# Performance work log

Hardware: AMD Instinct MI355X
Metric: run time of the kernel (lower is better)

Reference implementation:

```python
import jax, jax.numpy as jnp
import numpy as np

B, H, S, DK = 4, 16, 2048, 64


def setup_inputs() -> dict:
    key = jax.random.key(0)
    kq, kk, kv, km = jax.random.split(key, 4)
    Q = jax.random.normal(kq, (B, H, S, DK), dtype=jnp.float32)
    K = jax.random.normal(kk, (B, H, S, DK), dtype=jnp.float32)
    V = jax.random.normal(kv, (B, H, S, DK), dtype=jnp.float32)
    mask = (jax.random.uniform(km, (B, 1, S, S)) > 0.1).astype(jnp.float32)
    return {"Q": Q, "K": K, "V": V, "mask": mask}


def reference(Q, K, V, mask):
    d_k = Q.shape[-1]
    # unnormalized exp scores (no max subtraction), multiplicative mask
    scores = jnp.exp(jnp.einsum("bhqd,bhkd->bhqk", Q, K) / jnp.sqrt(jnp.float32(d_k)))
    scores = scores * mask
    attn = scores / (jnp.sum(scores, axis=-1, keepdims=True) + 1e-8)
    return jnp.einsum("bhqk,bhkd->bhqd", attn, V)
```

## Files before the change

kernel.cpp:

```cpp
#include <hip/hip_runtime.h>

namespace {
constexpr int S  = 2048;
constexpr int D  = 64;
constexpr int BQ = 128;
constexpr int BK = 64;
constexpr int NT = 512;
constexpr int NKT = S / BK;
constexpr int PSTR = 72;

typedef short bf16x8 __attribute__((ext_vector_type(8)));
typedef float f32x4  __attribute__((ext_vector_type(4)));

__device__ inline unsigned short bf16c(float x) {
  __bf16 h = (__bf16)x;
  return __builtin_bit_cast(unsigned short, h);
}
__device__ inline unsigned pk2(float a, float b) {
  return (unsigned)bf16c(a) | ((unsigned)bf16c(b) << 16);
}
__device__ inline void gld_lds16(const void* g, void* l) {
  __builtin_amdgcn_global_load_lds(
      (const __attribute__((address_space(1))) unsigned int*)g,
      (__attribute__((address_space(3))) unsigned int*)l, 16, 0, 0);
}

__global__ __launch_bounds__(256) void prep_k(const float* __restrict__ K,
                                              unsigned short* __restrict__ Kws) {
  int gid = blockIdx.x * 256 + threadIdx.x;
  int row = gid >> 3;
  int g   = gid & 7;
  const float* src = K + (size_t)row * 64 + g * 8;
  float4 a = *(const float4*)src;
  float4 b = *(const float4*)(src + 4);
  uint4 w;
  w.x = pk2(a.x, a.y); w.y = pk2(a.z, a.w);
  w.z = pk2(b.x, b.y); w.w = pk2(b.z, b.w);
  *(uint4*)(Kws + (size_t)row * 64 + ((g ^ (row & 7)) * 8)) = w;
}

__global__ __launch_bounds__(256) void prep_v(const float* __restrict__ V,
                                              unsigned short* __restrict__ Vws) {
  __shared__ float tl[64 * 68];
  const int t = threadIdx.x;
  const size_t tile = blockIdx.x;
  const float* src = V + tile * (64 * 64);
#pragma unroll
  for (int rep = 0; rep < 4; ++rep) {
    int idx = t + rep * 256;
    int row = idx >> 4, d4 = idx & 15;
    float4 v = *(const float4*)(src + row * 64 + d4 * 4);
    *(float4*)(tl + row * 68 + d4 * 4) = v;
  }
  __syncthreads();
  unsigned short* dstT = Vws + tile * (64 * 64);
#pragma unroll
  for (int rep = 0; rep < 2; ++rep) {
    int d  = (t & 31) + rep * 32;
    int kg = t >> 5;
    float x[8];
#pragma unroll
    for (int j = 0; j < 8; ++j) x[j] = tl[(kg * 8 + j) * 68 + d];
    uint4 w;
    w.x = pk2(x[0], x[1]); w.y = pk2(x[2], x[3]);
    w.z = pk2(x[4], x[5]); w.w = pk2(x[6], x[7]);
    *(uint4*)(dstT + d * 64 + ((kg ^ (d & 7)) * 8)) = w;
  }
}

__global__ __launch_bounds__(256) void prep_m(const float* __restrict__ M,
                                              unsigned char* __restrict__ M2) {
  size_t gid = (size_t)blockIdx.x * 256 + threadIdx.x;
  int n16  = gid & 15;
  int quad = (gid >> 4) & 3;
  size_t rest = gid >> 6;
  int qband = rest & 127;
  int kt    = (rest >> 7) & 31;
  int b     = rest >> 12;
  unsigned wds[4];
#pragma unroll
  for (int r = 0; r < 4; ++r) {
    int q = qband * 16 + quad * 4 + r;
    const float* src = M + ((size_t)b * S + q) * S + kt * 64 + n16;
    unsigned w = 0;
#pragma unroll
    for (int nt = 0; nt < 4; ++nt)
      w |= (src[nt * 16] != 0.0f ? 1u : 0u) << (8 * nt);
    wds[r] = w;
  }
  uint4 out = make_uint4(wds[0], wds[1], wds[2], wds[3]);
  *(uint4*)(M2 + gid * 16) = out;
}

__global__ __launch_bounds__(NT, 6)
void attn3(const float* __restrict__ Qg, const unsigned char* __restrict__ M2,
           const unsigned short* __restrict__ Kws,
           const unsigned short* __restrict__ Vws,
           float* __restrict__ Og) {
  __shared__ __align__(16) unsigned short sK[2][BK * D];
  __shared__ __align__(16) unsigned short sV[2][BK * D];
  __shared__ __align__(16) unsigned short sP[BQ * PSTR];

  const int t    = threadIdx.x;
  const int wave = t >> 6;
  const int lane = t & 63;
  const int quad = lane >> 4;
  const int n16  = lane & 15;

  const int bh = blockIdx.y;
  const int b  = bh >> 4;
  const int q0 = blockIdx.x * BQ;
  const int qband = blockIdx.x * 8 + wave;

  const unsigned short* Kb = Kws + (size_t)bh * S * D;
  const unsigned short* Vb = Vws + (size_t)bh * S * D;
  const unsigned char* Mp = M2
      + ((((size_t)b * NKT) * 128 + qband) * 4 + quad) * 256 + n16 * 16;
  constexpr size_t MKT = (size_t)128 * 4 * 16 * 16;

  const float* Qb = Qg + ((size_t)bh * S + q0 + wave * 16) * D;
  bf16x8 aq[2];
#pragma unroll
  for (int ks = 0; ks < 2; ++ks) {
    const float* qp = Qb + n16 * D + ks * 32 + quad * 8;
    float4 x = *(const float4*)qp;
    float4 y = *(const float4*)(qp + 4);
    bf16x8 a;
    a[0] = (short)bf16c(x.x * 0.125f); a[1] = (short)bf16c(x.y * 0.125f);
    a[2] = (short)bf16c(x.z * 0.125f); a[3] = (short)bf16c(x.w * 0.125f);
    a[4] = (short)bf16c(y.x * 0.125f); a[5] = (short)bf16c(y.y * 0.125f);
    a[6] = (short)bf16c(y.z * 0.125f); a[7] = (short)bf16c(y.w * 0.125f);
    aq[ks] = a;
  }

  f32x4 o[4];
#pragma unroll
  for (int nt = 0; nt < 4; ++nt) o[nt] = (f32x4){0.f, 0.f, 0.f, 0.f};
  float rs[4] = {0.f, 0.f, 0.f, 0.f};
  uint4 mk[2];

  gld_lds16(Kb + wave * 512 + lane * 8, &sK[0][wave * 512]);
  gld_lds16(Vb + wave * 512 + lane * 8, &sV[0][wave * 512]);
  mk[0] = *(const uint4*)Mp;

#pragma unroll 2
  for (int kt = 0; kt < NKT; ++kt) {
    const int cur = kt & 1, nxt = cur ^ 1;
    __syncthreads();

    if (kt + 1 < NKT) {
      gld_lds16(Kb + (size_t)(kt + 1) * (BK * D) + wave * 512 + lane * 8,
                &sK[nxt][wave * 512]);
      gld_lds16(Vb + (size_t)(kt + 1) * (BK * D) + wave * 512 + lane * 8,
                &sV[nxt][wave * 512]);
      mk[nxt] = *(const uint4*)(Mp + (size_t)(kt + 1) * MKT);
    }

    f32x4 sc[4];
#pragma unroll
    for (int nt = 0; nt < 4; ++nt) {
      const int row = nt * 16 + n16, sw = row & 7;
      bf16x8 bk0 = *(const bf16x8*)(sK[cur] + row * 64 + ((quad) ^ sw) * 8);
      bf16x8 bk1 = *(const bf16x8*)(sK[cur] + row * 64 + ((quad + 4) ^ sw) * 8);
      sc[nt] = (f32x4){0.f, 0.f, 0.f, 0.f};
      sc[nt] = __builtin_amdgcn_mfma_f32_16x16x32_bf16(aq[0], bk0, sc[nt], 0, 0, 0);
      sc[nt] = __builtin_amdgcn_mfma_f32_16x16x32_bf16(aq[1], bk1, sc[nt], 0, 0, 0);
    }

    const unsigned mw[4] = {mk[cur].x, mk[cur].y, mk[cur].z, mk[cur].w};
#pragma unroll
    for (int nt = 0; nt < 4; ++nt)
#pragma unroll
      for (int r = 0; r < 4; ++r) {
        float m = (float)((mw[r] >> (8 * nt)) & 0xffu);
        float p = __expf(sc[nt][r]) * m;
        unsigned short u = bf16c(p);
        rs[r] += __builtin_bit_cast(float, (unsigned)u << 16);
        sP[(wave * 16 + quad * 4 + r) * PSTR + nt * 16 + n16] = u;
      }

    const int prow = wave * 16 + n16;
    bf16x8 ap0 = *(const bf16x8*)(sP + prow * PSTR + quad * 8);
    bf16x8 ap1 = *(const bf16x8*)(sP + prow * PSTR + 32 + quad * 8);
#pragma unroll
    for (int nt = 0; nt < 4; ++nt) {
      const int row = nt * 16 + n16, sw = row & 7;
      bf16x8 bv0 = *(const bf16x8*)(sV[cur] + row * 64 + ((quad) ^ sw) * 8);
      bf16x8 bv1 = *(const bf16x8*)(sV[cur] + row * 64 + ((quad + 4) ^ sw) * 8);
      o[nt] = __builtin_amdgcn_mfma_f32_16x16x32_bf16(ap0, bv0, o[nt], 0, 0, 0);
      o[nt] = __builtin_amdgcn_mfma_f32_16x16x32_bf16(ap1, bv1, o[nt], 0, 0, 0);
    }
  }

  float inv[4];
#pragma unroll
  for (int r = 0; r < 4; ++r) {
    float v = rs[r];
    v += __shfl_xor(v, 1);
    v += __shfl_xor(v, 2);
    v += __shfl_xor(v, 4);
    v += __shfl_xor(v, 8);
    inv[r] = 1.0f / (v + 1e-8f);
  }
  float* Ob = Og + ((size_t)bh * S + q0 + wave * 16) * D;
#pragma unroll
  for (int nt = 0; nt < 4; ++nt)
#pragma unroll
    for (int r = 0; r < 4; ++r)
      Ob[(size_t)(quad * 4 + r) * D + nt * 16 + n16] = o[nt][r] * inv[r];
}
}

extern "C" void kernel_launch(void* const* d_in, const int* in_sizes, int n_in,
                              void* d_out, int out_size, void* d_ws, size_t ws_size,
                              hipStream_t stream) {
  const float* Q = (const float*)d_in[0];
  const float* K = (const float*)d_in[1];
  const float* V = (const float*)d_in[2];
  const float* M = (const float*)d_in[3];
  float* O = (float*)d_out;

  unsigned short* Kws = (unsigned short*)d_ws;
  unsigned short* Vws = Kws + (size_t)64 * S * D;
  unsigned char*  M2  = (unsigned char*)(Vws + (size_t)64 * S * D);

  prep_k<<<dim3(64 * S * D / 8 / 256), 256, 0, stream>>>(K, Kws);
  prep_v<<<dim3(64 * NKT), 256, 0, stream>>>(V, Vws);
  prep_m<<<dim3(4 * NKT * 128 * 4 * 16 / 256), 256, 0, stream>>>(M, M2);
  attn3<<<dim3(S / BQ, 64), NT, 0, stream>>>(Q, M2, Kws, Vws, O);
}
```

Baseline: 292.1 us.

## Compute transposed S^T tiles to keep P in registers and double rows per wave

Swaps the MFMA operand order so the score tile comes out transposed, which lets the exp'd probabilities be packed directly into MFMA A/B operands. This removes the shared-memory P round-trip. Each wave now handles 32 query rows (BQ=256), so every K/V fragment read from LDS is reused twice. Row sums come from an MFMA against a ones vector instead of a shuffle reduction. exp2 with a pre-scaled Q replaces __expf, and the K swizzle and mask packing are reorganized to match the new fragment layout. The costs are higher register pressure (occupancy hint lowered to 4), fewer blocks, and mask loads that are no longer prefetched a tile ahead.

```diff
diff --git a/kernel.cpp b/kernel.cpp
--- a/kernel.cpp
+++ b/kernel.cpp
@@ -3,11 +3,10 @@
 namespace {
 constexpr int S  = 2048;
 constexpr int D  = 64;
-constexpr int BQ = 128;
+constexpr int BQ = 256;
 constexpr int BK = 64;
 constexpr int NT = 512;
 constexpr int NKT = S / BK;
-constexpr int PSTR = 72;
 
 typedef short bf16x8 __attribute__((ext_vector_type(8)));
 typedef float f32x4  __attribute__((ext_vector_type(4)));
@@ -23,6 +22,28 @@
   __builtin_amdgcn_global_load_lds(
       (const __attribute__((address_space(1))) unsigned int*)g,
       (__attribute__((address_space(3))) unsigned int*)l, 16, 0, 0);
+}
+#if __has_builtin(__builtin_amdgcn_exp2f)
+__device__ inline float exp2v(float x) { return __builtin_amdgcn_exp2f(x); }
+#else
+__device__ inline float exp2v(float x) { return __expf(x * 0.6931471805599453f); }
+#endif
+
+__device__ inline int kswz_of_row(int row) {
+  return ((row >> 3) & 3) | ((row & 1) << 2);
+}
+
+__device__ inline bf16x8 mk_pa(f32x4 s0, f32x4 s1, unsigned mw0, unsigned mw1) {
+  float p0 = exp2v(s0[0]) * (float)(mw0 & 0xffu);
+  float p1 = exp2v(s0[1]) * (float)((mw0 >> 8) & 0xffu);
+  float p2 = exp2v(s0[2]) * (float)((mw0 >> 16) & 0xffu);
+  float p3 = exp2v(s0[3]) * (float)(mw0 >> 24);
+  float p4 = exp2v(s1[0]) * (float)(mw1 & 0xffu);
+  float p5 = exp2v(s1[1]) * (float)((mw1 >> 8) & 0xffu);
+  float p6 = exp2v(s1[2]) * (float)((mw1 >> 16) & 0xffu);
+  float p7 = exp2v(s1[3]) * (float)(mw1 >> 24);
+  uint4 u = make_uint4(pk2(p0, p1), pk2(p2, p3), pk2(p4, p5), pk2(p6, p7));
+  return __builtin_bit_cast(bf16x8, u);
 }
 
 __global__ __launch_bounds__(256) void prep_k(const float* __restrict__ K,
@@ -36,7 +57,7 @@
   uint4 w;
   w.x = pk2(a.x, a.y); w.y = pk2(a.z, a.w);
   w.z = pk2(b.x, b.y); w.w = pk2(b.z, b.w);
-  *(uint4*)(Kws + (size_t)row * 64 + ((g ^ (row & 7)) * 8)) = w;
+  *(uint4*)(Kws + (size_t)row * 64 + ((g ^ kswz_of_row(row)) * 8)) = w;
 }
 
 __global__ __launch_bounds__(256) void prep_v(const float* __restrict__ V,
@@ -71,35 +92,37 @@
 __global__ __launch_bounds__(256) void prep_m(const float* __restrict__ M,
                                               unsigned char* __restrict__ M2) {
   size_t gid = (size_t)blockIdx.x * 256 + threadIdx.x;
-  int n16  = gid & 15;
-  int quad = (gid >> 4) & 3;
-  size_t rest = gid >> 6;
-  int qband = rest & 127;
-  int kt    = (rest >> 7) & 31;
-  int b     = rest >> 12;
+  int g    = (int)(gid & 1);
+  int lane = (int)((gid >> 1) & 63);
+  int qg   = (int)((gid >> 7) & 63);
+  int kt   = (int)((gid >> 13) & 31);
+  int b    = (int)(gid >> 18);
+  int n16  = lane & 15;
+  int quad = (lane >> 4) & 3;
+  int q = qg * 32 + g * 16 + n16;
+  const float* src = M + ((size_t)b * S + q) * S + kt * 64 + quad * 8;
   unsigned wds[4];
 #pragma unroll
-  for (int r = 0; r < 4; ++r) {
-    int q = qband * 16 + quad * 4 + r;
-    const float* src = M + ((size_t)b * S + q) * S + kt * 64 + n16;
-    unsigned w = 0;
-#pragma unroll
-    for (int nt = 0; nt < 4; ++nt)
-      w |= (src[nt * 16] != 0.0f ? 1u : 0u) << (8 * nt);
-    wds[r] = w;
-  }
-  uint4 out = make_uint4(wds[0], wds[1], wds[2], wds[3]);
-  *(uint4*)(M2 + gid * 16) = out;
-}
-
-__global__ __launch_bounds__(NT, 6)
+  for (int w = 0; w < 4; ++w) {
+    int ks = w >> 1, h = w & 1;
+    float4 v = *(const float4*)(src + ks * 32 + h * 4);
+    unsigned m = 0;
+    if (v.x != 0.0f) m |= 0x00000001u;
+    if (v.y != 0.0f) m |= 0x00000100u;
+    if (v.z != 0.0f) m |= 0x00010000u;
+    if (v.w != 0.0f) m |= 0x01000000u;
+    wds[w] = m;
+  }
+  *(uint4*)(M2 + gid * 16) = make_uint4(wds[0], wds[1], wds[2], wds[3]);
+}
+
+__global__ __launch_bounds__(NT, 4)
 void attn3(const float* __restrict__ Qg, const unsigned char* __restrict__ M2,
            const unsigned short* __restrict__ Kws,
            const unsigned short* __restrict__ Vws,
            float* __restrict__ Og) {
   __shared__ __align__(16) unsigned short sK[2][BK * D];
   __shared__ __align__(16) unsigned short sV[2][BK * D];
-  __shared__ __align__(16) unsigned short sP[BQ * PSTR];
 
   const int t    = threadIdx.x;
   const int wave = t >> 6;
@@ -110,104 +133,131 @@
   const int bh = blockIdx.y;
   const int b  = bh >> 4;
   const int q0 = blockIdx.x * BQ;
-  const int qband = blockIdx.x * 8 + wave;
+  const int qg = blockIdx.x * 8 + wave;
 
   const unsigned short* Kb = Kws + (size_t)bh * S * D;
   const unsigned short* Vb = Vws + (size_t)bh * S * D;
-  const unsigned char* Mp = M2
-      + ((((size_t)b * NKT) * 128 + qband) * 4 + quad) * 256 + n16 * 16;
-  constexpr size_t MKT = (size_t)128 * 4 * 16 * 16;
-
-  const float* Qb = Qg + ((size_t)bh * S + q0 + wave * 16) * D;
-  bf16x8 aq[2];
+  const unsigned char* Mp = M2 + (((size_t)b * NKT * 64 + qg) * 64 + lane) * 32;
+  constexpr size_t MKT = (size_t)64 * 64 * 32;
+
+  const int h2 = n16 >> 2, rr = n16 & 3;
+  const int kswz  = h2 | ((rr & 1) << 2);
+  const int koffA = (quad ^ kswz) * 8;
+  const int koffB = ((quad + 4) ^ kswz) * 8;
+  const int krow0 = (8 * h2 + rr) * 64;
+
+  const int sw = n16 & 7;
+  const int ga = (quad ^ sw) * 8;
+  const int gb = ((quad + 4) ^ sw) * 8;
+
+  constexpr float QS = 0.18033688011112042f;
+  const float* QbA = Qg + ((size_t)bh * S + q0 + wave * 32 + n16) * D;
+  bf16x8 aqA[2], aqB[2];
 #pragma unroll
   for (int ks = 0; ks < 2; ++ks) {
-    const float* qp = Qb + n16 * D + ks * 32 + quad * 8;
+    const float* qp = QbA + ks * 32 + quad * 8;
     float4 x = *(const float4*)qp;
     float4 y = *(const float4*)(qp + 4);
     bf16x8 a;
-    a[0] = (short)bf16c(x.x * 0.125f); a[1] = (short)bf16c(x.y * 0.125f);
-    a[2] = (short)bf16c(x.z * 0.125f); a[3] = (short)bf16c(x.w * 0.125f);
-    a[4] = (short)bf16c(y.x * 0.125f); a[5] = (short)bf16c(y.y * 0.125f);
-    a[6] = (short)bf16c(y.z * 0.125f); a[7] = (short)bf16c(y.w * 0.125f);
-    aq[ks] = a;
-  }
-
-  f32x4 o[4];
-#pragma unroll
-  for (int nt = 0; nt < 4; ++nt) o[nt] = (f32x4){0.f, 0.f, 0.f, 0.f};
-  float rs[4] = {0.f, 0.f, 0.f, 0.f};
-  uint4 mk[2];
+    a[0] = (short)bf16c(x.x * QS); a[1] = (short)bf16c(x.y * QS);
+    a[2] = (short)bf16c(x.z * QS); a[3] = (short)bf16c(x.w * QS);
+    a[4] = (short)bf16c(y.x * QS); a[5] = (short)bf16c(y.y * QS);
+    a[6] = (short)bf16c(y.z * QS); a[7] = (short)bf16c(y.w * QS);
+    aqA[ks] = a;
+    const float* qp2 = qp + 16 * D;
+    float4 x2 = *(const float4*)qp2;
+    float4 y2 = *(const float4*)(qp2 + 4);
+    bf16x8 a2;
+    a2[0] = (short)bf16c(x2.x * QS); a2[1] = (short)bf16c(x2.y * QS);
+    a2[2] = (short)bf16c(x2.z * QS); a2[3] = (short)bf16c(x2.w * QS);
+    a2[4] = (short)bf16c(y2.x * QS); a2[5] = (short)bf16c(y2.y * QS);
+    a2[6] = (short)bf16c(y2.z * QS); a2[7] = (short)bf16c(y2.w * QS);
+    aqB[ks] = a2;
+  }
+
+  bf16x8 ones;
+#pragma unroll
+  for (int i = 0; i < 8; ++i) ones[i] = (short)0x3F80;
+
+  f32x4 oA[4], oB[4];
+#pragma unroll
+  for (int nt = 0; nt < 4; ++nt) {
+    oA[nt] = (f32x4){0.f, 0.f, 0.f, 0.f};
+    oB[nt] = (f32x4){0.f, 0.f, 0.f, 0.f};
+  }
+  f32x4 rsA = (f32x4){0.f, 0.f, 0.f, 0.f};
+  f32x4 rsB = (f32x4){0.f, 0.f, 0.f, 0.f};
 
   gld_lds16(Kb + wave * 512 + lane * 8, &sK[0][wave * 512]);
   gld_lds16(Vb + wave * 512 + lane * 8, &sV[0][wave * 512]);
-  mk[0] = *(const uint4*)Mp;
 
 #pragma unroll 2
   for (int kt = 0; kt < NKT; ++kt) {
     const int cur = kt & 1, nxt = cur ^ 1;
     __syncthreads();
+
+    uint4 mkA = *(const uint4*)(Mp + (size_t)kt * MKT);
+    uint4 mkB = *(const uint4*)(Mp + (size_t)kt * MKT + 16);
 
     if (kt + 1 < NKT) {
       gld_lds16(Kb + (size_t)(kt + 1) * (BK * D) + wave * 512 + lane * 8,
                 &sK[nxt][wave * 512]);
       gld_lds16(Vb + (size_t)(kt + 1) * (BK * D) + wave * 512 + lane * 8,
                 &sV[nxt][wave * 512]);
-      mk[nxt] = *(const uint4*)(Mp + (size_t)(kt + 1) * MKT);
     }
 
-    f32x4 sc[4];
+    bf16x8 paA[2], paB[2];
+#pragma unroll
+    for (int ks = 0; ks < 2; ++ks) {
+      const unsigned short* base = &sK[cur][krow0 + ks * 2048];
+      bf16x8 k0a = *(const bf16x8*)(base + koffA);
+      bf16x8 k0b = *(const bf16x8*)(base + koffB);
+      bf16x8 k1a = *(const bf16x8*)(base + 256 + koffA);
+      bf16x8 k1b = *(const bf16x8*)(base + 256 + koffB);
+      const f32x4 z = (f32x4){0.f, 0.f, 0.f, 0.f};
+
+      f32x4 sA0 = __builtin_amdgcn_mfma_f32_16x16x32_bf16(k0a, aqA[0], z, 0, 0, 0);
+      sA0 = __builtin_amdgcn_mfma_f32_16x16x32_bf16(k0b, aqA[1], sA0, 0, 0, 0);
+      f32x4 sA1 = __builtin_amdgcn_mfma_f32_16x16x32_bf16(k1a, aqA[0], z, 0, 0, 0);
+      sA1 = __builtin_amdgcn_mfma_f32_16x16x32_bf16(k1b, aqA[1], sA1, 0, 0, 0);
+      paA[ks] = mk_pa(sA0, sA1, ks ? mkA.z : mkA.x, ks ? mkA.w : mkA.y);
+
+      f32x4 sB0 = __builtin_amdgcn_mfma_f32_16x16x32_bf16(k0a, aqB[0], z, 0, 0, 0);
+      sB0 = __builtin_amdgcn_mfma_f32_16x16x32_bf16(k0b, aqB[1], sB0, 0, 0, 0);
+      f32x4 sB1 = __builtin_amdgcn_mfma_f32_16x16x32_bf16(k1a, aqB[0], z, 0, 0, 0);
+      sB1 = __builtin_amdgcn_mfma_f32_16x16x32_bf16(k1b, aqB[1], sB1, 0, 0, 0);
+      paB[ks] = mk_pa(sB0, sB1, ks ? mkB.z : mkB.x, ks ? mkB.w : mkB.y);
+    }
+
+    rsA = __builtin_amdgcn_mfma_f32_16x16x32_bf16(ones, paA[0], rsA, 0, 0, 0);
+    rsA = __builtin_amdgcn_mfma_f32_16x16x32_bf16(ones, paA[1], rsA, 0, 0, 0);
+    rsB = __builtin_amdgcn_mfma_f32_16x16x32_bf16(ones, paB[0], rsB, 0, 0, 0);
+    rsB = __builtin_amdgcn_mfma_f32_16x16x32_bf16(ones, paB[1], rsB, 0, 0, 0);
+
 #pragma unroll
     for (int nt = 0; nt < 4; ++nt) {
-      const int row = nt * 16 + n16, sw = row & 7;
-      bf16x8 bk0 = *(const bf16x8*)(sK[cur] + row * 64 + ((quad) ^ sw) * 8);
-      bf16x8 bk1 = *(const bf16x8*)(sK[cur] + row * 64 + ((quad + 4) ^ sw) * 8);
-      sc[nt] = (f32x4){0.f, 0.f, 0.f, 0.f};
-      sc[nt] = __builtin_amdgcn_mfma_f32_16x16x32_bf16(aq[0], bk0, sc[nt], 0, 0, 0);
-      sc[nt] = __builtin_amdgcn_mfma_f32_16x16x32_bf16(aq[1], bk1, sc[nt], 0, 0, 0);
+      const int row = nt * 16 + n16;
+      bf16x8 v0 = *(const bf16x8*)(sV[cur] + row * 64 + ga);
+      bf16x8 v1 = *(const bf16x8*)(sV[cur] + row * 64 + gb);
+      oA[nt] = __builtin_amdgcn_mfma_f32_16x16x32_bf16(v0, paA[0], oA[nt], 0, 0, 0);
+      oA[nt] = __builtin_amdgcn_mfma_f32_16x16x32_bf16(v1, paA[1], oA[nt], 0, 0, 0);
+      oB[nt] = __builtin_amdgcn_mfma_f32_16x16x32_bf16(v0, paB[0], oB[nt], 0, 0, 0);
+      oB[nt] = __builtin_amdgcn_mfma_f32_16x16x32_bf16(v1, paB[1], oB[nt], 0, 0, 0);
     }
-
-    const unsigned mw[4] = {mk[cur].x, mk[cur].y, mk[cur].z, mk[cur].w};
-#pragma unroll
-    for (int nt = 0; nt < 4; ++nt)
-#pragma unroll
-      for (int r = 0; r < 4; ++r) {
-        float m = (float)((mw[r] >> (8 * nt)) & 0xffu);
-        float p = __expf(sc[nt][r]) * m;
-        unsigned short u = bf16c(p);
-        rs[r] += __builtin_bit_cast(float, (unsigned)u << 16);
-        sP[(wave * 16 + quad * 4 + r) * PSTR + nt * 16 + n16] = u;
-      }
-
-    const int prow = wave * 16 + n16;
-    bf16x8 ap0 = *(const bf16x8*)(sP + prow * PSTR + quad * 8);
-    bf16x8 ap1 = *(const bf16x8*)(sP + prow * PSTR + 32 + quad * 8);
-#pragma unroll
-    for (int nt = 0; nt < 4; ++nt) {
-      const int row = nt * 16 + n16, sw = row & 7;
-      bf16x8 bv0 = *(const bf16x8*)(sV[cur] + row * 64 + ((quad) ^ sw) * 8);
-      bf16x8 bv1 = *(const bf16x8*)(sV[cur] + row * 64 + ((quad + 4) ^ sw) * 8);
-      o[nt] = __builtin_amdgcn_mfma_f32_16x16x32_bf16(ap0, bv0, o[nt], 0, 0, 0);
-      o[nt] = __builtin_amdgcn_mfma_f32_16x16x32_bf16(ap1, bv1, o[nt], 0, 0, 0);
-    }
-  }
-
-  float inv[4];
-#pragma unroll
-  for (int r = 0; r < 4; ++r) {
-    float v = rs[r];
-    v += __shfl_xor(v, 1);
-    v += __shfl_xor(v, 2);
-    v += __shfl_xor(v, 4);
-    v += __shfl_xor(v, 8);
-    inv[r] = 1.0f / (v + 1e-8f);
-  }
-  float* Ob = Og + ((size_t)bh * S + q0 + wave * 16) * D;
-#pragma unroll
-  for (int nt = 0; nt < 4; ++nt)
-#pragma unroll
-    for (int r = 0; r < 4; ++r)
-      Ob[(size_t)(quad * 4 + r) * D + nt * 16 + n16] = o[nt][r] * inv[r];
+  }
+
+  const float invA = 1.0f / (rsA[0] + 1e-8f);
+  const float invB = 1.0f / (rsB[0] + 1e-8f);
+  float* OA = Og + ((size_t)bh * S + q0 + wave * 32 + n16) * D;
+#pragma unroll
+  for (int nt = 0; nt < 4; ++nt) {
+    float4 wa = make_float4(oA[nt][0] * invA, oA[nt][1] * invA,
+                            oA[nt][2] * invA, oA[nt][3] * invA);
+    *(float4*)(OA + nt * 16 + quad * 4) = wa;
+    float4 wb = make_float4(oB[nt][0] * invB, oB[nt][1] * invB,
+                            oB[nt][2] * invB, oB[nt][3] * invB);
+    *(float4*)(OA + 16 * D + nt * 16 + quad * 4) = wb;
+  }
 }
 }
 
@@ -226,6 +276,6 @@
 
   prep_k<<<dim3(64 * S * D / 8 / 256), 256, 0, stream>>>(K, Kws);
   prep_v<<<dim3(64 * NKT), 256, 0, stream>>>(V, Vws);
-  prep_m<<<dim3(4 * NKT * 128 * 4 * 16 / 256), 256, 0, stream>>>(M, M2);
+  prep_m<<<dim3(4 * NKT * 64 * 64 * 2 / 256), 256, 0, stream>>>(M, M2);
   attn3<<<dim3(S / BQ, 64), NT, 0, stream>>>(Q, M2, Kws, Vws, O);
 }
```

Measured after the change: 270.7 us. 1.08x faster.
